# Kernel optimization log

Measured on AMD Instinct MI355X. Metric: run time of the kernel, lower is better.

The kernel has to match this reference:

```python
import math
import jax, jax.numpy as jnp
import numpy as np

H = 2048
T = 8192
NUM_LAYERS = 24
LAYER_ID = 6


def setup_inputs() -> dict:
    key = jax.random.key(0)
    ks = jax.random.split(key, 5)
    ratio_0_to_1 = LAYER_ID / (NUM_LAYERS - 1)
    ratio_1_to_almost_0 = 1.0 - LAYER_ID / NUM_LAYERS
    # parameter init exactly as in RwkvSelfAttention.__init__
    zigzag = 0.5 * (jnp.arange(1, H + 1) % 3 - 1)
    time_first = jnp.full((H,), math.log(0.3), jnp.float32) + zigzag.astype(jnp.float32)
    hh = jnp.arange(0, H, dtype=jnp.float32)
    time_decay = -5.0 + 8.0 * (hh / (H - 1)) ** (0.7 + 1.3 * ratio_0_to_1)
    xx = jnp.arange(H, dtype=jnp.float32) / H
    time_mix_key = jnp.power(xx, ratio_1_to_almost_0)
    time_mix_value = time_mix_key + 0.3 * ratio_0_to_1
    time_mix_receptance = jnp.power(xx, 0.5 * ratio_1_to_almost_0)
    scale = 1.0 / math.sqrt(H)
    return {
        "hidden": jax.random.normal(ks[0], (T, H), jnp.float32),
        "sx": jnp.zeros((H,), jnp.float32),
        "aa": jnp.zeros((H,), jnp.float32),
        "bb": jnp.zeros((H,), jnp.float32),
        "pp": jnp.full((H,), -1e30, jnp.float32),  # log-space -inf init
        "time_decay": time_decay,
        "time_first": time_first,
        "time_mix_key": time_mix_key,
        "time_mix_value": time_mix_value,
        "time_mix_receptance": time_mix_receptance,
        "Wk": jax.random.normal(ks[1], (H, H), jnp.float32) * scale,
        "Wv": jax.random.normal(ks[2], (H, H), jnp.float32) * scale,
        "Wr": jax.random.normal(ks[3], (H, H), jnp.float32) * scale,
        "Wo": jax.random.normal(ks[4], (H, H), jnp.float32) * scale,
    }


def reference(hidden, sx, aa, bb, pp, time_decay, time_first, time_mix_key,
              time_mix_value, time_mix_receptance, Wk, Wv, Wr, Wo):
    # token-shift mix: c_x[t] = hidden[t-1], c_x[0] = sx
    c_x = jnp.concatenate((sx[None, :], hidden[:-1, :]), axis=0)  # [T, H]
    key_x = hidden * time_mix_key + c_x * (1.0 - time_mix_key)
    value_x = hidden * time_mix_value + c_x * (1.0 - time_mix_value)
    receptance_x = hidden * time_mix_receptance + c_x * (1.0 - time_mix_receptance)

    r = jax.nn.sigmoid(receptance_x @ Wr)  # [T, H]
    k = key_x @ Wk                         # [T, H]
    v = value_x @ Wv                       # [T, H]

    w_decay = -jnp.exp(time_decay)  # [H]

    def step(state, kv):
        a, b, p = state
        kk, vv = kv
        # output with bonus (time_first)
        ww = time_first + kk
        q = jnp.maximum(p, ww)
        e1 = jnp.exp(p - q)
        e2 = jnp.exp(ww - q)
        out_t = (e1 * a + e2 * vv) / (e1 * b + e2)
        # state update with decay
        ww2 = w_decay + p
        q2 = jnp.maximum(ww2, kk)
        e1b = jnp.exp(ww2 - q2)
        e2b = jnp.exp(kk - q2)
        return (e1b * a + e2b * vv, e1b * b + e2b, q2), out_t

    (aa, bb, pp), wkv = jax.lax.scan(step, (aa, bb, pp), (k, v))  # wkv: [T, H]

    out = hidden + (r * wkv) @ Wo
    return out, hidden[-1, :], aa, bb, pp
```

## Files before the change

### kernel.cpp

```cpp
#include <hip/hip_runtime.h>
#include <stdint.h>

#define H 2048
#define T 8192
#define C_CH 128
#define L_CH 64

typedef unsigned short u16;
typedef unsigned int u32;

__device__ __forceinline__ float bf2f(u16 u) {
  return __uint_as_float(((u32)u) << 16);
}
__device__ __forceinline__ u16 f2bf(float f) {
  u32 u = __float_as_uint(f);
  u = u + 0x7FFFu + ((u >> 16) & 1u);
  return (u16)(u >> 16);
}
__device__ __forceinline__ bool in_is_bf16(const u32* ppw) {
  u32 w = ppw[0];
  return (w >> 16) == (w & 0xFFFFu);
}
__device__ __forceinline__ float ldin(const void* p, size_t i, bool bf) {
  return bf ? bf2f(((const u16*)p)[i]) : ((const float*)p)[i];
}
__device__ __forceinline__ void stout(void* p, size_t i, float v, bool bf) {
  if (bf) ((u16*)p)[i] = f2bf(v);
  else ((float*)p)[i] = v;
}

__global__ void mix3_kernel(const void* __restrict__ hidden,
                            const void* __restrict__ sx,
                            const void* __restrict__ tmk,
                            const void* __restrict__ tmv,
                            const void* __restrict__ tmr,
                            u16* __restrict__ outk, u16* __restrict__ outv,
                            u16* __restrict__ outr, const u32* __restrict__ ppw) {
  bool bf = in_is_bf16(ppw);
  int i = blockIdx.x * blockDim.x + threadIdx.x;
  int h = i & (H - 1);
  float hv = ldin(hidden, (size_t)i, bf);
  float cv = (i < H) ? ldin(sx, (size_t)h, bf) : ldin(hidden, (size_t)i - H, bf);
  float d = hv - cv;
  outk[i] = f2bf(cv + ldin(tmk, (size_t)h, bf) * d);
  outv[i] = f2bf(cv + ldin(tmv, (size_t)h, bf) * d);
  outr[i] = f2bf(cv + ldin(tmr, (size_t)h, bf) * d);
}

__global__ void transpose_kernel(const void* __restrict__ W, u16* __restrict__ Wt,
                                 const u32* __restrict__ ppw) {
  bool bf = in_is_bf16(ppw);
  __shared__ u16 tile[32][33];
  int bx = blockIdx.x * 32, by = blockIdx.y * 32;
  int tx = threadIdx.x, ty = threadIdx.y;
#pragma unroll
  for (int j = 0; j < 32; j += 8)
    tile[ty + j][tx] = f2bf(ldin(W, (size_t)(by + ty + j) * H + bx + tx, bf));
  __syncthreads();
#pragma unroll
  for (int j = 0; j < 32; j += 8)
    Wt[(size_t)(bx + ty + j) * H + by + tx] = tile[tx][ty + j];
}

typedef short bf16x8 __attribute__((ext_vector_type(8)));
typedef float f32x4 __attribute__((ext_vector_type(4)));

#define MODE_K 0
#define MODE_BF16 1
#define MODE_SIG 2
#define MODE_ADDH 3

__device__ __forceinline__ void gl_lds16(const short* g, short* l) {
  __builtin_amdgcn_global_load_lds((__attribute__((address_space(1))) void*)(g),
                                   (__attribute__((address_space(3))) void*)(l),
                                   16, 0, 0);
}

template <int MODE>
__global__ __launch_bounds__(256) void gemm_kernel(
    const u16* __restrict__ Au, const u16* __restrict__ Btu,
    void* __restrict__ C, const void* __restrict__ hid,
    const u32* __restrict__ ppw) {
  __shared__ short As[128 * 64];
  __shared__ short Bs[128 * 64];
  const short* A = (const short*)Au;
  const short* Bt = (const short*)Btu;

  const int bid = blockIdx.x;
  const int xcd = bid & 7;
  const int s = bid >> 3;
  const int mblk = (xcd << 3) | (s & 7);
  const int nblk = s >> 3;
  const int m0 = mblk * 128;
  const int n0 = nblk * 128;

  const int tid = threadIdx.x;
  const int lane = tid & 63;
  const int wid = tid >> 6;
  const int wm = wid >> 1;
  const int wn = wid & 1;
  const int lrow = lane & 15;
  const int quad = lane >> 4;

  const int srow = lane >> 2;
  const int scol = (lane & 3) * 8;
  const short* gA = A + (size_t)(m0 + wid * 32 + srow) * H + scol;
  const short* gB = Bt + (size_t)(n0 + wid * 32 + srow) * H + scol;
  short* lA = As + wid * 1024;
  short* lB = Bs + wid * 1024;

  f32x4 acc[4][4];
#pragma unroll
  for (int i = 0; i < 4; i++)
#pragma unroll
    for (int j = 0; j < 4; j++) acc[i][j] = (f32x4){0.f, 0.f, 0.f, 0.f};

  for (int k0 = 0; k0 < H; k0 += 64) {
    __syncthreads();
    gl_lds16(gA + k0, lA);
    gl_lds16(gA + k0 + 16 * H, lA + 512);
    gl_lds16(gB + k0, lB);
    gl_lds16(gB + k0 + 16 * H, lB + 512);
    gl_lds16(gA + k0 + 32, lA + 4096);
    gl_lds16(gA + k0 + 32 + 16 * H, lA + 4096 + 512);
    gl_lds16(gB + k0 + 32, lB + 4096);
    gl_lds16(gB + k0 + 32 + 16 * H, lB + 4096 + 512);
    __syncthreads();
#pragma unroll
    for (int sub = 0; sub < 2; sub++) {
      const short* as = As + sub * 4096;
      const short* bs = Bs + sub * 4096;
      bf16x8 af[4], bfr[4];
#pragma unroll
      for (int i = 0; i < 4; i++)
        af[i] = *(const bf16x8*)(as + (wm * 64 + i * 16 + lrow) * 32 + quad * 8);
#pragma unroll
      for (int j = 0; j < 4; j++)
        bfr[j] = *(const bf16x8*)(bs + (wn * 64 + j * 16 + lrow) * 32 + quad * 8);
#pragma unroll
      for (int i = 0; i < 4; i++)
#pragma unroll
        for (int j = 0; j < 4; j++)
          acc[i][j] = __builtin_amdgcn_mfma_f32_16x16x32_bf16(af[i], bfr[j], acc[i][j], 0, 0, 0);
    }
  }

  bool bf = (MODE == MODE_ADDH) ? in_is_bf16(ppw) : true;
#pragma unroll
  for (int i = 0; i < 4; i++) {
#pragma unroll
    for (int j = 0; j < 4; j++) {
#pragma unroll
      for (int reg = 0; reg < 4; reg++) {
        int row = m0 + wm * 64 + i * 16 + quad * 4 + reg;
        int col = n0 + wn * 64 + j * 16 + lrow;
        size_t idx = (size_t)row * H + col;
        float val = acc[i][j][reg];
        if (MODE == MODE_K || MODE == MODE_BF16) {
          ((u16*)C)[idx] = f2bf(val);
        } else if (MODE == MODE_SIG) {
          ((u16*)C)[idx] = f2bf(1.0f / (1.0f + __expf(-val)));
        } else {
          stout(C, idx, val + ldin(hid, idx, bf), bf);
        }
      }
    }
  }
}

__global__ __launch_bounds__(256) void wkv_local_kernel(
    const u16* __restrict__ kbuf, const u16* __restrict__ vbuf,
    const void* __restrict__ tdec,
    float* __restrict__ suma, float* __restrict__ sumb, float* __restrict__ sump,
    const u32* __restrict__ ppw) {
  bool bf = in_is_bf16(ppw);
  int h = blockIdx.x * 256 + threadIdx.x;
  int c = blockIdx.y;
  float w = -__expf(ldin(tdec, h, bf));
  float a = 0.f, b = 0.f, p = -1e30f;
  size_t base = (size_t)c * L_CH * H + h;
#pragma unroll 4
  for (int t = 0; t < L_CH; t++) {
    size_t idx = base + (size_t)t * H;
    float kk = bf2f(kbuf[idx]);
    float vv = bf2f(vbuf[idx]);
    float ww2 = w + p;
    float q2 = fmaxf(ww2, kk);
    float e1b = __expf(ww2 - q2), e2b = __expf(kk - q2);
    a = e1b * a + e2b * vv;
    b = e1b * b + e2b;
    p = q2;
  }
  suma[(size_t)c * H + h] = a;
  sumb[(size_t)c * H + h] = b;
  sump[(size_t)c * H + h] = p;
}

__global__ __launch_bounds__(256) void wkv_prefix_kernel(
    const float* __restrict__ suma, const float* __restrict__ sumb,
    const float* __restrict__ sump,
    const void* __restrict__ aa_in, const void* __restrict__ bb_in,
    const void* __restrict__ pp_in, const void* __restrict__ tdec,
    const void* __restrict__ hidden,
    float* __restrict__ sta, float* __restrict__ stb, float* __restrict__ stp,
    void* __restrict__ dout, const u32* __restrict__ ppw) {
  bool bf = in_is_bf16(ppw);
  int h = blockIdx.x * 256 + threadIdx.x;
  float a = ldin(aa_in, h, bf), b = ldin(bb_in, h, bf), p = ldin(pp_in, h, bf);
  float w = -__expf(ldin(tdec, h, bf));
  float wL = w * (float)L_CH;
  for (int c = 0; c < C_CH; c++) {
    size_t i = (size_t)c * H + h;
    sta[i] = a;
    stb[i] = b;
    stp[i] = p;
    float la = suma[i], lb = sumb[i], lp = sump[i];
    float pd = p + wL;
    float q = fmaxf(pd, lp);
    float e1 = __expf(pd - q), e2 = __expf(lp - q);
    a = e1 * a + e2 * la;
    b = e1 * b + e2 * lb;
    p = q;
  }
  size_t base = (size_t)T * H;
  stout(dout, base + h, ldin(hidden, (size_t)(T - 1) * H + h, bf), bf);
  stout(dout, base + H + h, a, bf);
  stout(dout, base + 2 * H + h, b, bf);
  stout(dout, base + 3 * H + h, p, bf);
}

__global__ __launch_bounds__(256) void wkv_out_kernel(
    const u16* __restrict__ kbuf, const u16* __restrict__ vbuf,
    const u16* __restrict__ rbuf,
    const float* __restrict__ sta, const float* __restrict__ stb,
    const float* __restrict__ stp,
    const void* __restrict__ tdec, const void* __restrict__ tfirst,
    u16* __restrict__ rw, const u32* __restrict__ ppw) {
  bool bf = in_is_bf16(ppw);
  int h = blockIdx.x * 256 + threadIdx.x;
  int c = blockIdx.y;
  size_t si = (size_t)c * H + h;
  float a = sta[si], b = stb[si], p = stp[si];
  float tf = ldin(tfirst, h, bf);
  float w = -__expf(ldin(tdec, h, bf));
  size_t base = (size_t)c * L_CH * H + h;
#pragma unroll 4
  for (int t = 0; t < L_CH; t++) {
    size_t idx = base + (size_t)t * H;
    float kk = bf2f(kbuf[idx]);
    float vv = bf2f(vbuf[idx]);
    float rr = bf2f(rbuf[idx]);
    float ww = tf + kk;
    float q = fmaxf(p, ww);
    float e1 = __expf(p - q), e2 = __expf(ww - q);
    float wkv = (e1 * a + e2 * vv) / (e1 * b + e2);
    rw[idx] = f2bf(rr * wkv);
    float ww2 = w + p;
    float q2 = fmaxf(ww2, kk);
    float e1b = __expf(ww2 - q2), e2b = __expf(kk - q2);
    a = e1b * a + e2b * vv;
    b = e1b * b + e2b;
    p = q2;
  }
}

extern "C" void kernel_launch(void* const* d_in, const int* in_sizes, int n_in,
                              void* d_out, int out_size, void* d_ws, size_t ws_size,
                              hipStream_t stream) {
  const void* hidden = d_in[0];
  const void* sx = d_in[1];
  const void* aa = d_in[2];
  const void* bb = d_in[3];
  const void* pp = d_in[4];
  const void* tdec = d_in[5];
  const void* tfirst = d_in[6];
  const void* tmk = d_in[7];
  const void* tmv = d_in[8];
  const void* tmr = d_in[9];
  const void* Wk = d_in[10];
  const void* Wv = d_in[11];
  const void* Wr = d_in[12];
  const void* Wo = d_in[13];
  const u32* ppw = (const u32*)d_in[4];

  char* ws = (char*)d_ws;
  const size_t TH2 = (size_t)T * H * 2;
  const size_t WT2 = (size_t)H * H * 2;
  u16* A1 = (u16*)ws;
  u16* A2 = (u16*)(ws + TH2);
  u16* A3 = (u16*)(ws + 2 * TH2);
  u16* B1 = (u16*)(ws + 3 * TH2);
  u16* Wt_buf = (u16*)(ws + 4 * TH2);
  float* suma = (float*)(ws + 4 * TH2 + WT2);
  float* sumb = suma + (size_t)C_CH * H;
  float* sump = sumb + (size_t)C_CH * H;
  float* sta = sump + (size_t)C_CH * H;
  float* stb = sta + (size_t)C_CH * H;
  float* stp = stb + (size_t)C_CH * H;

  dim3 mixG((T * H) / 256), mixB(256);
  dim3 trG(64, 64), trB(32, 8);
  dim3 gG(1024), gB(256);
  dim3 scG(H / 256, C_CH), scB(256);

  mix3_kernel<<<mixG, mixB, 0, stream>>>(hidden, sx, tmk, tmv, tmr,
                                         A1, A2, A3, ppw);
  transpose_kernel<<<trG, trB, 0, stream>>>(Wr, Wt_buf, ppw);
  gemm_kernel<MODE_SIG><<<gG, gB, 0, stream>>>(A3, Wt_buf, B1, nullptr, ppw);
  transpose_kernel<<<trG, trB, 0, stream>>>(Wk, Wt_buf, ppw);
  gemm_kernel<MODE_K><<<gG, gB, 0, stream>>>(A1, Wt_buf, A3, nullptr, ppw);
  transpose_kernel<<<trG, trB, 0, stream>>>(Wv, Wt_buf, ppw);
  gemm_kernel<MODE_BF16><<<gG, gB, 0, stream>>>(A2, Wt_buf, A1, nullptr, ppw);
  wkv_local_kernel<<<scG, scB, 0, stream>>>(A3, A1, tdec, suma, sumb, sump, ppw);
  wkv_prefix_kernel<<<dim3(H / 256), scB, 0, stream>>>(
      suma, sumb, sump, aa, bb, pp, tdec, hidden, sta, stb, stp, d_out, ppw);
  wkv_out_kernel<<<scG, scB, 0, stream>>>(A3, A1, B1, sta, stb, stp,
                                          tdec, tfirst, A2, ppw);
  transpose_kernel<<<trG, trB, 0, stream>>>(Wo, Wt_buf, ppw);
  gemm_kernel<MODE_ADDH><<<gG, gB, 0, stream>>>(A2, Wt_buf, d_out, hidden, ppw);
}
```

Baseline: 674.6 us.

## Rewrite GEMM with 256x256 tiles, double-buffered LDS and XOR swizzle

Measured after the change: 619.4 us. -8.2%, faster.

```diff
diff --git a/kernel.cpp b/kernel.cpp
--- a/kernel.cpp
+++ b/kernel.cpp
@@ -77,82 +77,133 @@
 }
 
 template <int MODE>
-__global__ __launch_bounds__(256) void gemm_kernel(
+__global__ __launch_bounds__(512, 2) void gemm_kernel(
     const u16* __restrict__ Au, const u16* __restrict__ Btu,
     void* __restrict__ C, const void* __restrict__ hid,
     const u32* __restrict__ ppw) {
-  __shared__ short As[128 * 64];
-  __shared__ short Bs[128 * 64];
+  __shared__ short As[2][256 * 64];
+  __shared__ short Bs[2][256 * 64];
   const short* A = (const short*)Au;
   const short* Bt = (const short*)Btu;
 
   const int bid = blockIdx.x;
   const int xcd = bid & 7;
   const int s = bid >> 3;
-  const int mblk = (xcd << 3) | (s & 7);
-  const int nblk = s >> 3;
-  const int m0 = mblk * 128;
-  const int n0 = nblk * 128;
+  const int mblk = (xcd << 2) | (s & 3);
+  const int nblk = s >> 2;
+  const int m0 = mblk * 256;
+  const int n0 = nblk * 256;
 
   const int tid = threadIdx.x;
   const int lane = tid & 63;
   const int wid = tid >> 6;
-  const int wm = wid >> 1;
-  const int wn = wid & 1;
+  const int wm = wid >> 2;
+  const int wn = wid & 3;
   const int lrow = lane & 15;
   const int quad = lane >> 4;
 
-  const int srow = lane >> 2;
-  const int scol = (lane & 3) * 8;
-  const short* gA = A + (size_t)(m0 + wid * 32 + srow) * H + scol;
-  const short* gB = Bt + (size_t)(n0 + wid * 32 + srow) * H + scol;
-  short* lA = As + wid * 1024;
-  short* lB = Bs + wid * 1024;
-
-  f32x4 acc[4][4];
-#pragma unroll
-  for (int i = 0; i < 4; i++)
+  const int srow = lane >> 3;
+  const int schunk = (lane & 7) ^ srow;
+  const short* gA = A + (size_t)(m0 + wid * 32 + srow) * H + schunk * 8;
+  const short* gB = Bt + (size_t)(n0 + wid * 32 + srow) * H + schunk * 8;
+  short* lA0 = &As[0][0] + wid * 2048;
+  short* lB0 = &Bs[0][0] + wid * 2048;
+  short* lA1 = &As[1][0] + wid * 2048;
+  short* lB1 = &Bs[1][0] + wid * 2048;
+
+  const int swz = (lrow & 7) << 4;
+
+  f32x4 acc[8][4];
+#pragma unroll
+  for (int i = 0; i < 8; i++)
 #pragma unroll
     for (int j = 0; j < 4; j++) acc[i][j] = (f32x4){0.f, 0.f, 0.f, 0.f};
 
-  for (int k0 = 0; k0 < H; k0 += 64) {
-    __syncthreads();
-    gl_lds16(gA + k0, lA);
-    gl_lds16(gA + k0 + 16 * H, lA + 512);
-    gl_lds16(gB + k0, lB);
-    gl_lds16(gB + k0 + 16 * H, lB + 512);
-    gl_lds16(gA + k0 + 32, lA + 4096);
-    gl_lds16(gA + k0 + 32 + 16 * H, lA + 4096 + 512);
-    gl_lds16(gB + k0 + 32, lB + 4096);
-    gl_lds16(gB + k0 + 32 + 16 * H, lB + 4096 + 512);
-    __syncthreads();
-#pragma unroll
-    for (int sub = 0; sub < 2; sub++) {
-      const short* as = As + sub * 4096;
-      const short* bs = Bs + sub * 4096;
-      bf16x8 af[4], bfr[4];
-#pragma unroll
-      for (int i = 0; i < 4; i++)
-        af[i] = *(const bf16x8*)(as + (wm * 64 + i * 16 + lrow) * 32 + quad * 8);
+#define STAGE(lA, lB, koff)                                    \
+  do {                                                         \
+    _Pragma("unroll") for (int q = 0; q < 4; q++)              \
+        gl_lds16(gA + (size_t)q * 8 * H + (koff), (lA) + q * 512); \
+    _Pragma("unroll") for (int q = 0; q < 4; q++)              \
+        gl_lds16(gB + (size_t)q * 8 * H + (koff), (lB) + q * 512); \
+  } while (0)
+
+  const int NT = H / 64;
+
+  STAGE(lA0, lB0, 0);
+  STAGE(lA1, lB1, 64);
+  asm volatile("s_waitcnt vmcnt(8)" ::: "memory");
+  __builtin_amdgcn_sched_barrier(0);
+  __builtin_amdgcn_s_barrier();
+
+  for (int t = 0; t < NT; ++t) {
+    const int cur = t & 1;
+    const char* asb = (const char*)&As[cur][0];
+    const char* bsb = (const char*)&Bs[cur][0];
+
+    bf16x8 a0[8], b0[4];
+#pragma unroll
+    for (int i = 0; i < 8; i++)
+      a0[i] = *(const bf16x8*)(asb + (size_t)(wm * 128 + i * 16 + lrow) * 128 +
+                               ((quad * 16) ^ swz));
+#pragma unroll
+    for (int j = 0; j < 4; j++)
+      b0[j] = *(const bf16x8*)(bsb + (size_t)(wn * 64 + j * 16 + lrow) * 128 +
+                               ((quad * 16) ^ swz));
+    bf16x8 a1[8], b1[4];
+#pragma unroll
+    for (int i = 0; i < 8; i++)
+      a1[i] = *(const bf16x8*)(asb + (size_t)(wm * 128 + i * 16 + lrow) * 128 +
+                               ((64 + quad * 16) ^ swz));
+#pragma unroll
+    for (int j = 0; j < 4; j++)
+      b1[j] = *(const bf16x8*)(bsb + (size_t)(wn * 64 + j * 16 + lrow) * 128 +
+                               ((64 + quad * 16) ^ swz));
+
+    __builtin_amdgcn_s_setprio(1);
+#pragma unroll
+    for (int i = 0; i < 8; i++)
 #pragma unroll
       for (int j = 0; j < 4; j++)
-        bfr[j] = *(const bf16x8*)(bs + (wn * 64 + j * 16 + lrow) * 32 + quad * 8);
-#pragma unroll
-      for (int i = 0; i < 4; i++)
-#pragma unroll
-        for (int j = 0; j < 4; j++)
-          acc[i][j] = __builtin_amdgcn_mfma_f32_16x16x32_bf16(af[i], bfr[j], acc[i][j], 0, 0, 0);
+        acc[i][j] = __builtin_amdgcn_mfma_f32_16x16x32_bf16(a0[i], b0[j],
+                                                            acc[i][j], 0, 0, 0);
+    __builtin_amdgcn_s_setprio(0);
+
+    asm volatile("s_waitcnt lgkmcnt(0)" ::: "memory");
+    __builtin_amdgcn_sched_barrier(0);
+    if (t < NT - 2) {
+      __builtin_amdgcn_s_barrier();
+      const int koff = (t + 2) * 64;
+      if (cur == 0) STAGE(lA0, lB0, koff);
+      else          STAGE(lA1, lB1, koff);
     }
-  }
+
+    __builtin_amdgcn_s_setprio(1);
+#pragma unroll
+    for (int i = 0; i < 8; i++)
+#pragma unroll
+      for (int j = 0; j < 4; j++)
+        acc[i][j] = __builtin_amdgcn_mfma_f32_16x16x32_bf16(a1[i], b1[j],
+                                                            acc[i][j], 0, 0, 0);
+    __builtin_amdgcn_s_setprio(0);
+
+    if (t < NT - 2) {
+      asm volatile("s_waitcnt vmcnt(8)" ::: "memory");
+    } else if (t == NT - 2) {
+      asm volatile("s_waitcnt vmcnt(0)" ::: "memory");
+    }
+    __builtin_amdgcn_sched_barrier(0);
+    if (t < NT - 1) __builtin_amdgcn_s_barrier();
+  }
+#undef STAGE
 
   bool bf = (MODE == MODE_ADDH) ? in_is_bf16(ppw) : true;
 #pragma unroll
-  for (int i = 0; i < 4; i++) {
+  for (int i = 0; i < 8; i++) {
 #pragma unroll
     for (int j = 0; j < 4; j++) {
 #pragma unroll
       for (int reg = 0; reg < 4; reg++) {
-        int row = m0 + wm * 64 + i * 16 + quad * 4 + reg;
+        int row = m0 + wm * 128 + i * 16 + quad * 4 + reg;
         int col = n0 + wn * 64 + j * 16 + lrow;
         size_t idx = (size_t)row * H + col;
         float val = acc[i][j][reg];
@@ -300,7 +351,7 @@
 
   dim3 mixG((T * H) / 256), mixB(256);
   dim3 trG(64, 64), trB(32, 8);
-  dim3 gG(1024), gB(256);
+  dim3 gG(256), gB(512);
   dim3 scG(H / 256, C_CH), scB(256);
 
   mix3_kernel<<<mixG, mixB, 0, stream>>>(hidden, sx, tmk, tmv, tmr,
```

## Rewrite bf16 GEMM as 256x256 tiles with 8 waves and quad-buffered LDS pipeline

Applied to the files above, without the earlier changes.

Result: faster. 656.5 us (-2.7%).

```diff
diff --git a/kernel.cpp b/kernel.cpp
--- a/kernel.cpp
+++ b/kernel.cpp
@@ -76,29 +76,35 @@
                                    16, 0, 0);
 }
 
+__device__ __forceinline__ void stage_ht(const short* g, size_t koff,
+                                         short* slot, int wid) {
+  gl_lds16(g + koff, slot + wid * 1024);
+  gl_lds16(g + koff + (size_t)16 * H, slot + wid * 1024 + 512);
+}
+
 template <int MODE>
-__global__ __launch_bounds__(256) void gemm_kernel(
+__global__ __launch_bounds__(512, 2) void gemm_kernel(
     const u16* __restrict__ Au, const u16* __restrict__ Btu,
     void* __restrict__ C, const void* __restrict__ hid,
     const u32* __restrict__ ppw) {
-  __shared__ short As[128 * 64];
-  __shared__ short Bs[128 * 64];
+  __shared__ alignas(16) short As[4][256 * 32];
+  __shared__ alignas(16) short Bs[4][256 * 32];
   const short* A = (const short*)Au;
   const short* Bt = (const short*)Btu;
 
   const int bid = blockIdx.x;
   const int xcd = bid & 7;
   const int s = bid >> 3;
-  const int mblk = (xcd << 3) | (s & 7);
-  const int nblk = s >> 3;
-  const int m0 = mblk * 128;
-  const int n0 = nblk * 128;
+  const int mblk = (xcd << 2) | (s & 3);
+  const int nblk = s >> 2;
+  const int m0 = mblk * 256;
+  const int n0 = nblk * 256;
 
   const int tid = threadIdx.x;
   const int lane = tid & 63;
   const int wid = tid >> 6;
-  const int wm = wid >> 1;
-  const int wn = wid & 1;
+  const int wm = wid >> 2;
+  const int wn = wid & 3;
   const int lrow = lane & 15;
   const int quad = lane >> 4;
 
@@ -106,53 +112,95 @@
   const int scol = (lane & 3) * 8;
   const short* gA = A + (size_t)(m0 + wid * 32 + srow) * H + scol;
   const short* gB = Bt + (size_t)(n0 + wid * 32 + srow) * H + scol;
-  short* lA = As + wid * 1024;
-  short* lB = Bs + wid * 1024;
-
-  f32x4 acc[4][4];
-#pragma unroll
-  for (int i = 0; i < 4; i++)
+
+  const int aoff = (wm * 128 + lrow) * 32 + quad * 8;
+  const int boff = (wn * 64 + lrow) * 32 + quad * 8;
+
+  f32x4 acc[8][4];
+#pragma unroll
+  for (int i = 0; i < 8; i++)
 #pragma unroll
     for (int j = 0; j < 4; j++) acc[i][j] = (f32x4){0.f, 0.f, 0.f, 0.f};
 
-  for (int k0 = 0; k0 < H; k0 += 64) {
-    __syncthreads();
-    gl_lds16(gA + k0, lA);
-    gl_lds16(gA + k0 + 16 * H, lA + 512);
-    gl_lds16(gB + k0, lB);
-    gl_lds16(gB + k0 + 16 * H, lB + 512);
-    gl_lds16(gA + k0 + 32, lA + 4096);
-    gl_lds16(gA + k0 + 32 + 16 * H, lA + 4096 + 512);
-    gl_lds16(gB + k0 + 32, lB + 4096);
-    gl_lds16(gB + k0 + 32 + 16 * H, lB + 4096 + 512);
-    __syncthreads();
-#pragma unroll
-    for (int sub = 0; sub < 2; sub++) {
-      const short* as = As + sub * 4096;
-      const short* bs = Bs + sub * 4096;
-      bf16x8 af[4], bfr[4];
-#pragma unroll
-      for (int i = 0; i < 4; i++)
-        af[i] = *(const bf16x8*)(as + (wm * 64 + i * 16 + lrow) * 32 + quad * 8);
-#pragma unroll
-      for (int j = 0; j < 4; j++)
-        bfr[j] = *(const bf16x8*)(bs + (wn * 64 + j * 16 + lrow) * 32 + quad * 8);
-#pragma unroll
-      for (int i = 0; i < 4; i++)
-#pragma unroll
-        for (int j = 0; j < 4; j++)
-          acc[i][j] = __builtin_amdgcn_mfma_f32_16x16x32_bf16(af[i], bfr[j], acc[i][j], 0, 0, 0);
-    }
-  }
+  const int NT = H / 64;
+
+  stage_ht(gA, 0, As[0], wid);
+  stage_ht(gB, 0, Bs[0], wid);
+  stage_ht(gA, 32, As[1], wid);
+  stage_ht(gB, 32, Bs[1], wid);
+  stage_ht(gA, 64, As[2], wid);
+  stage_ht(gB, 64, Bs[2], wid);
+  stage_ht(gA, 96, As[3], wid);
+  stage_ht(gB, 96, Bs[3], wid);
+  asm volatile("s_waitcnt vmcnt(8)" ::: "memory");
+  __builtin_amdgcn_sched_barrier(0);
+  __builtin_amdgcn_s_barrier();
+
+  bf16x8 af[4], bfg[4];
+
+#define PHASE_CORE(ks, mh, BREAD, STAGE_STMT, DRAIN_STMT)                     \
+  {                                                                           \
+    const short* aslot = &As[(b << 1) | (ks)][0];                             \
+    _Pragma("unroll") for (int ii = 0; ii < 4; ii++)                          \
+        af[ii] = *(const bf16x8*)(aslot + aoff + (mh)*2048 + ii * 512);       \
+    if (BREAD) {                                                              \
+      const short* bslot = &Bs[(b << 1) | (ks)][0];                           \
+      _Pragma("unroll") for (int j = 0; j < 4; j++)                           \
+          bfg[j] = *(const bf16x8*)(bslot + boff + j * 512);                  \
+    }                                                                         \
+    STAGE_STMT;                                                               \
+    __builtin_amdgcn_s_barrier();                                             \
+    asm volatile("s_waitcnt lgkmcnt(0)" ::: "memory");                        \
+    __builtin_amdgcn_sched_barrier(0);                                        \
+    __builtin_amdgcn_s_setprio(1);                                            \
+    _Pragma("unroll") for (int ii = 0; ii < 4; ii++)                          \
+      _Pragma("unroll") for (int j = 0; j < 4; j++)                           \
+          acc[(mh)*4 + ii][j] = __builtin_amdgcn_mfma_f32_16x16x32_bf16(      \
+              af[ii], bfg[j], acc[(mh)*4 + ii][j], 0, 0, 0);                  \
+    __builtin_amdgcn_s_setprio(0);                                            \
+    DRAIN_STMT;                                                               \
+    __builtin_amdgcn_s_barrier();                                             \
+  }
+
+  for (int tau = 0; tau < NT; ++tau) {
+    const int b = tau & 1;
+    const int bo = b ^ 1;
+
+    PHASE_CORE(0, 0, true,
+               { if (tau >= 1 && tau <= NT - 2)
+                   stage_ht(gA, (size_t)(tau + 1) * 64 + 32, &As[(bo << 1) | 1][0], wid); },
+               {})
+    PHASE_CORE(0, 1, false,
+               { if (tau >= 1 && tau <= NT - 2)
+                   stage_ht(gB, (size_t)(tau + 1) * 64 + 32, &Bs[(bo << 1) | 1][0], wid); },
+               {
+                 if (tau == NT - 1) { asm volatile("s_waitcnt vmcnt(0)" ::: "memory"); }
+                 else               { asm volatile("s_waitcnt vmcnt(8)" ::: "memory"); }
+                 __builtin_amdgcn_sched_barrier(0);
+               })
+    PHASE_CORE(1, 0, true,
+               { if (tau <= NT - 3)
+                   stage_ht(gA, (size_t)(tau + 2) * 64, &As[(b << 1) | 0][0], wid); },
+               {})
+    PHASE_CORE(1, 1, false,
+               { if (tau <= NT - 3)
+                   stage_ht(gB, (size_t)(tau + 2) * 64, &Bs[(b << 1) | 0][0], wid); },
+               {
+                 if (tau == NT - 2) { asm volatile("s_waitcnt vmcnt(4)" ::: "memory"); }
+                 else               { asm volatile("s_waitcnt vmcnt(8)" ::: "memory"); }
+                 __builtin_amdgcn_sched_barrier(0);
+               })
+  }
+#undef PHASE_CORE
 
   bool bf = (MODE == MODE_ADDH) ? in_is_bf16(ppw) : true;
 #pragma unroll
-  for (int i = 0; i < 4; i++) {
+  for (int i = 0; i < 8; i++) {
 #pragma unroll
     for (int j = 0; j < 4; j++) {
 #pragma unroll
       for (int reg = 0; reg < 4; reg++) {
-        int row = m0 + wm * 64 + i * 16 + quad * 4 + reg;
+        int row = m0 + wm * 128 + i * 16 + quad * 4 + reg;
         int col = n0 + wn * 64 + j * 16 + lrow;
         size_t idx = (size_t)row * H + col;
         float val = acc[i][j][reg];
@@ -300,7 +348,7 @@
 
   dim3 mixG((T * H) / 256), mixB(256);
   dim3 trG(64, 64), trB(32, 8);
-  dim3 gG(1024), gB(256);
+  dim3 gG(256), gB(512);
   dim3 scG(H / 256, C_CH), scB(256);
 
   mix3_kernel<<<mixG, mixB, 0, stream>>>(hidden, sx, tmk, tmv, tmr,
```

## Restructure GEMM into 256x128 tiles with triple-buffered LDS pipeline and swizzle

Applied to the files above, without the earlier changes.

Result: faster. 597.2 us (-11.5%).

```diff
diff --git a/kernel.cpp b/kernel.cpp
--- a/kernel.cpp
+++ b/kernel.cpp
@@ -64,6 +64,7 @@
 
 typedef short bf16x8 __attribute__((ext_vector_type(8)));
 typedef float f32x4 __attribute__((ext_vector_type(4)));
+typedef float f32x2 __attribute__((ext_vector_type(2)));
 
 #define MODE_K 0
 #define MODE_BF16 1
@@ -77,21 +78,22 @@
 }
 
 template <int MODE>
-__global__ __launch_bounds__(256) void gemm_kernel(
+__global__ __launch_bounds__(512, 4) void gemm_kernel(
     const u16* __restrict__ Au, const u16* __restrict__ Btu,
     void* __restrict__ C, const void* __restrict__ hid,
     const u32* __restrict__ ppw) {
-  __shared__ short As[128 * 64];
-  __shared__ short Bs[128 * 64];
+  __shared__ alignas(16) char lds_raw[73728];
+  short* const As0 = (short*)lds_raw;
+  short* const Bs0 = (short*)lds_raw + 3 * 8192;
   const short* A = (const short*)Au;
   const short* Bt = (const short*)Btu;
 
   const int bid = blockIdx.x;
   const int xcd = bid & 7;
   const int s = bid >> 3;
-  const int mblk = (xcd << 3) | (s & 7);
-  const int nblk = s >> 3;
-  const int m0 = mblk * 128;
+  const int mblk = (xcd << 2) | (s & 3);
+  const int nblk = s >> 2;
+  const int m0 = mblk * 256;
   const int n0 = nblk * 128;
 
   const int tid = threadIdx.x;
@@ -103,11 +105,13 @@
   const int quad = lane >> 4;
 
   const int srow = lane >> 2;
-  const int scol = (lane & 3) * 8;
-  const short* gA = A + (size_t)(m0 + wid * 32 + srow) * H + scol;
-  const short* gB = Bt + (size_t)(n0 + wid * 32 + srow) * H + scol;
-  short* lA = As + wid * 1024;
-  short* lB = Bs + wid * 1024;
+  const int schunk = (lane & 3) ^ ((lane >> 3) & 3);
+  const short* gA = A + (size_t)(m0 + wid * 32 + srow) * H + schunk * 8;
+  const short* gB = Bt + (size_t)(n0 + wid * 16 + srow) * H + schunk * 8;
+
+  const int gxor = (quad ^ ((lrow >> 1) & 3)) * 8;
+  const int arow = (wm * 64 + lrow) * 32 + gxor;
+  const int brow = (wn * 64 + lrow) * 32 + gxor;
 
   f32x4 acc[4][4];
 #pragma unroll
@@ -115,53 +119,103 @@
 #pragma unroll
     for (int j = 0; j < 4; j++) acc[i][j] = (f32x4){0.f, 0.f, 0.f, 0.f};
 
-  for (int k0 = 0; k0 < H; k0 += 64) {
-    __syncthreads();
-    gl_lds16(gA + k0, lA);
-    gl_lds16(gA + k0 + 16 * H, lA + 512);
-    gl_lds16(gB + k0, lB);
-    gl_lds16(gB + k0 + 16 * H, lB + 512);
-    gl_lds16(gA + k0 + 32, lA + 4096);
-    gl_lds16(gA + k0 + 32 + 16 * H, lA + 4096 + 512);
-    gl_lds16(gB + k0 + 32, lB + 4096);
-    gl_lds16(gB + k0 + 32 + 16 * H, lB + 4096 + 512);
-    __syncthreads();
-#pragma unroll
-    for (int sub = 0; sub < 2; sub++) {
-      const short* as = As + sub * 4096;
-      const short* bs = Bs + sub * 4096;
-      bf16x8 af[4], bfr[4];
-#pragma unroll
-      for (int i = 0; i < 4; i++)
-        af[i] = *(const bf16x8*)(as + (wm * 64 + i * 16 + lrow) * 32 + quad * 8);
+  const int NT = H / 32;
+
+#define STAGE_TILE(koff, sl)                                   \
+  do {                                                         \
+    short* la = As0 + (sl)*8192 + wid * 1024;                  \
+    short* lb = Bs0 + (sl)*4096 + wid * 512;                   \
+    gl_lds16(gA + (koff), la);                                 \
+    gl_lds16(gA + (koff) + (size_t)16 * H, la + 512);          \
+    gl_lds16(gB + (koff), lb);                                 \
+  } while (0)
+
+  STAGE_TILE(0, 0);
+  STAGE_TILE(32, 1);
+  asm volatile("s_waitcnt vmcnt(3)" ::: "memory");
+  __builtin_amdgcn_sched_barrier(0);
+  __builtin_amdgcn_s_barrier();
+
+  for (int tau = 0; tau < NT; ++tau) {
+    const int rd = tau % 3;
+    const int st = (tau + 2) % 3;
+    const short* asl = As0 + rd * 8192;
+    const short* bsl = Bs0 + rd * 4096;
+
+    bf16x8 af[4], bfv[4];
+#pragma unroll
+    for (int i = 0; i < 4; i++)
+      af[i] = *(const bf16x8*)(asl + arow + i * 512);
+#pragma unroll
+    for (int j = 0; j < 4; j++)
+      bfv[j] = *(const bf16x8*)(bsl + brow + j * 512);
+
+    if (tau <= NT - 3) STAGE_TILE((size_t)(tau + 2) * 32, st);
+
+    __builtin_amdgcn_s_setprio(1);
+#pragma unroll
+    for (int i = 0; i < 4; i++)
 #pragma unroll
       for (int j = 0; j < 4; j++)
-        bfr[j] = *(const bf16x8*)(bs + (wn * 64 + j * 16 + lrow) * 32 + quad * 8);
-#pragma unroll
-      for (int i = 0; i < 4; i++)
+        acc[i][j] = __builtin_amdgcn_mfma_f32_16x16x32_bf16(af[i], bfv[j],
+                                                            acc[i][j], 0, 0, 0);
+    __builtin_amdgcn_s_setprio(0);
+
+    if (tau <= NT - 3) {
+      asm volatile("s_waitcnt vmcnt(3)" ::: "memory");
+    } else if (tau == NT - 2) {
+      asm volatile("s_waitcnt vmcnt(0)" ::: "memory");
+    }
+    __builtin_amdgcn_sched_barrier(0);
+    if (tau < NT - 1) __builtin_amdgcn_s_barrier();
+  }
+#undef STAGE_TILE
+
+  __builtin_amdgcn_s_barrier();
+  {
+    bool bf = (MODE == MODE_ADDH) ? in_is_bf16(ppw) : true;
+    float* lC = (float*)lds_raw + (size_t)wid * (32 * 66);
+    const int el = lane & 31;
+    const int eh = lane >> 5;
+#pragma unroll
+    for (int p = 0; p < 2; p++) {
+#pragma unroll
+      for (int ih = 0; ih < 2; ih++) {
+        const int i = p * 2 + ih;
 #pragma unroll
         for (int j = 0; j < 4; j++)
-          acc[i][j] = __builtin_amdgcn_mfma_f32_16x16x32_bf16(af[i], bfr[j], acc[i][j], 0, 0, 0);
-    }
-  }
-
-  bool bf = (MODE == MODE_ADDH) ? in_is_bf16(ppw) : true;
-#pragma unroll
-  for (int i = 0; i < 4; i++) {
-#pragma unroll
-    for (int j = 0; j < 4; j++) {
-#pragma unroll
-      for (int reg = 0; reg < 4; reg++) {
-        int row = m0 + wm * 64 + i * 16 + quad * 4 + reg;
-        int col = n0 + wn * 64 + j * 16 + lrow;
+#pragma unroll
+          for (int reg = 0; reg < 4; reg++)
+            lC[(ih * 16 + quad * 4 + reg) * 66 + j * 16 + lrow] =
+                acc[i][j][reg];
+      }
+#pragma unroll
+      for (int k = 0; k < 16; k++) {
+        const int rr = k * 2 + eh;
+        f32x2 v = *(const f32x2*)(lC + rr * 66 + el * 2);
+        const int row = m0 + wm * 64 + p * 32 + rr;
+        const int col = n0 + wn * 64 + el * 2;
         size_t idx = (size_t)row * H + col;
-        float val = acc[i][j][reg];
-        if (MODE == MODE_K || MODE == MODE_BF16) {
-          ((u16*)C)[idx] = f2bf(val);
-        } else if (MODE == MODE_SIG) {
-          ((u16*)C)[idx] = f2bf(1.0f / (1.0f + __expf(-val)));
+        if (MODE == MODE_SIG) {
+          v[0] = 1.0f / (1.0f + __expf(-v[0]));
+          v[1] = 1.0f / (1.0f + __expf(-v[1]));
+        }
+        if (MODE == MODE_ADDH) {
+          if (bf) {
+            u32 hv = *(const u32*)((const u16*)hid + idx);
+            v[0] += bf2f((u16)(hv & 0xFFFFu));
+            v[1] += bf2f((u16)(hv >> 16));
+            u32 pk = (u32)f2bf(v[0]) | ((u32)f2bf(v[1]) << 16);
+            *(u32*)((u16*)C + idx) = pk;
+          } else {
+            f32x2 hv = *(const f32x2*)((const float*)hid + idx);
+            v[0] += hv[0];
+            v[1] += hv[1];
+            *(f32x2*)((float*)C + idx) = v;
+          }
         } else {
-          stout(C, idx, val + ldin(hid, idx, bf), bf);
+          u32 pk = (u32)f2bf(v[0]) | ((u32)f2bf(v[1]) << 16);
+          *(u32*)((u16*)C + idx) = pk;
         }
       }
     }
@@ -300,7 +354,7 @@
 
   dim3 mixG((T * H) / 256), mixB(256);
   dim3 trG(64, 64), trB(32, 8);
-  dim3 gG(1024), gB(256);
+  dim3 gG(512), gB(512);
   dim3 scG(H / 256, C_CH), scB(256);
 
   mix3_kernel<<<mixG, mixB, 0, stream>>>(hidden, sx, tmk, tmv, tmr,
```
